# Kernel tuning notes

Hardware: AMD Instinct MI355X
Metric: run time of the kernel (lower is better)

## Reference

```python
import jax, jax.numpy as jnp
import numpy as np

B, T, D = 2, 2048, 2048
NH, HD = 16, 128
Q_LAT, KV_LAT = 1024, 512
EPS = 1e-6
THETA = 10000.0


def setup_inputs() -> dict:
    key = jax.random.key(0)
    ks = jax.random.split(key, 8)
    x = jax.random.normal(ks[0], (B, T, D), dtype=jnp.float32)
    # causal additive mask, broadcast over batch/heads
    neg = jnp.finfo(jnp.float32).min
    causal = jnp.where(jnp.tril(jnp.ones((T, T), dtype=bool)), 0.0, neg)
    attn_mask = causal[None, None, :, :].astype(jnp.float32)
    s = lambda fan_in: 1.0 / np.sqrt(fan_in)
    q_a_w = jax.random.normal(ks[1], (Q_LAT, D), dtype=jnp.float32) * s(D)
    q_b_w = jax.random.normal(ks[2], (NH * HD, Q_LAT), dtype=jnp.float32) * s(Q_LAT)
    kv_a_w = jax.random.normal(ks[3], (KV_LAT, D), dtype=jnp.float32) * s(D)
    k_b_w = jax.random.normal(ks[4], (NH * HD, KV_LAT), dtype=jnp.float32) * s(KV_LAT)
    v_b_w = jax.random.normal(ks[5], (NH * HD, KV_LAT), dtype=jnp.float32) * s(KV_LAT)
    o_w = jax.random.normal(ks[6], (D, NH * HD), dtype=jnp.float32) * s(NH * HD)
    q_norm_w = jnp.ones((HD,), dtype=jnp.float32)
    k_norm_w = jnp.ones((HD,), dtype=jnp.float32)
    return dict(x=x, attn_mask=attn_mask, q_a_w=q_a_w, q_b_w=q_b_w, kv_a_w=kv_a_w,
                k_b_w=k_b_w, v_b_w=v_b_w, o_w=o_w, q_norm_w=q_norm_w, k_norm_w=k_norm_w)


def _rms_norm(x, w):
    var = jnp.mean(jnp.square(x), axis=-1, keepdims=True)
    return x * jax.lax.rsqrt(var + EPS) * w


def _rope_cache(t, hd, dtype):
    inv_freq = 1.0 / (THETA ** (jnp.arange(0, hd, 2, dtype=jnp.float32) / hd))
    freqs = jnp.arange(t, dtype=jnp.float32)[:, None] * inv_freq[None, :]  # [t, hd/2]
    emb = jnp.concatenate([freqs, freqs], axis=-1)  # [t, hd]
    return jnp.cos(emb).astype(dtype), jnp.sin(emb).astype(dtype)


def _rotate_half(x):
    h = x.shape[-1] // 2
    return jnp.concatenate([-x[..., h:], x[..., :h]], axis=-1)


def reference(x, attn_mask, q_a_w, q_b_w, kv_a_w, k_b_w, v_b_w, o_w, q_norm_w, k_norm_w):
    b, t, d = x.shape
    # low-rank projections (torch Linear: y = x @ W.T)
    q = (x @ q_a_w.T) @ q_b_w.T          # [b, t, nh*hd]
    kv = x @ kv_a_w.T                     # [b, t, kv_lat]
    k = kv @ k_b_w.T
    v = kv @ v_b_w.T
    q = q.reshape(b, t, NH, HD).transpose(0, 2, 1, 3)  # [b, nh, t, hd]
    k = k.reshape(b, t, NH, HD).transpose(0, 2, 1, 3)
    v = v.reshape(b, t, NH, HD).transpose(0, 2, 1, 3)
    # QK-norm over head dim
    q = _rms_norm(q, q_norm_w)
    k = _rms_norm(k, k_norm_w)
    # RoPE
    cos, sin = _rope_cache(t, HD, x.dtype)  # [t, hd]
    cos = cos[None, None, :, :]
    sin = sin[None, None, :, :]
    q = q * cos + _rotate_half(q) * sin
    k = k * cos + _rotate_half(k) * sin
    # attention
    sd = 1.0 / np.sqrt(HD)
    attn = jnp.einsum('bhqd,bhkd->bhqk', q, k) * sd + attn_mask
    attn = jax.nn.softmax(attn, axis=-1)
    out = jnp.einsum('bhqk,bhkd->bhqd', attn, v)
    out = out.transpose(0, 2, 1, 3).reshape(b, t, NH * HD)
    return out @ o_w.T
```

## Files before the change

kernel.cpp:

```cpp
#include <hip/hip_runtime.h>
#include <hip/hip_fp16.h>

typedef _Float16 f16;
typedef _Float16 f16x4 __attribute__((ext_vector_type(4)));
typedef _Float16 f16x8 __attribute__((ext_vector_type(8)));
typedef float f32x4 __attribute__((ext_vector_type(4)));

#define BT 4096
#define DMODEL 2048

__device__ __forceinline__ void gld16(const f16* g, f16* l) {
    __builtin_amdgcn_global_load_lds((const __attribute__((address_space(1))) void*)g,
                                     (__attribute__((address_space(3))) void*)l, 16, 0, 0);
}

struct Cvt7 {
    const float* s[7];
    f16* d[7];
    int off4[8];
};
__global__ __launch_bounds__(256) void k_cvt7(Cvt7 c) {
    int i = blockIdx.x * 256 + threadIdx.x;
    if (i >= c.off4[7]) return;
    int seg = 0;
#pragma unroll
    for (int k = 1; k < 7; ++k) seg += (i >= c.off4[k]);
    int j = i - c.off4[seg];
    float4 v = ((const float4*)c.s[seg])[j];
    f16x4 h;
    h[0] = (f16)v.x; h[1] = (f16)v.y; h[2] = (f16)v.z; h[3] = (f16)v.w;
    ((f16x4*)c.d[seg])[j] = h;
}

template <typename CT>
__global__ __launch_bounds__(256, 3) void k_gemm_bt(const f16* __restrict__ A,
                                                    const f16* __restrict__ Bm,
                                                    CT* __restrict__ C,
                                                    int M, int N, int K) {
    __shared__ __align__(16) char smem[16384];
    f16* Als = (f16*)smem;
    f16* Bls = (f16*)(smem + 8192);
    const int tid = threadIdx.x;
    const int w = tid >> 6, l = tid & 63;
    const int quad = l >> 4, ln = l & 15;
    const int m0 = blockIdx.y * 128, n0 = blockIdx.x * 128;
    const int wm = (w >> 1) * 64, wn = (w & 1) * 64;
    const int srow = l >> 2, scol = (l & 3) * 8;

    f32x4 acc[4][4];
#pragma unroll
    for (int i = 0; i < 4; ++i)
#pragma unroll
        for (int j = 0; j < 4; ++j)
#pragma unroll
            for (int r = 0; r < 4; ++r) acc[i][j][r] = 0.f;

    for (int k0 = 0; k0 < K; k0 += 32) {
#pragma unroll
        for (int c = 0; c < 2; ++c) {
            const int ch = w + 4 * c;
            gld16(A + (size_t)(m0 + ch * 16 + srow) * K + (k0 + scol), &Als[ch * 512]);
            gld16(Bm + (size_t)(n0 + ch * 16 + srow) * K + (k0 + scol), &Bls[ch * 512]);
        }
        __syncthreads();
        f16x8 af[4], bf[4];
#pragma unroll
        for (int i = 0; i < 4; ++i) af[i] = *(const f16x8*)&Als[(wm + 16 * i + ln) * 32 + quad * 8];
#pragma unroll
        for (int j = 0; j < 4; ++j) bf[j] = *(const f16x8*)&Bls[(wn + 16 * j + ln) * 32 + quad * 8];
#pragma unroll
        for (int i = 0; i < 4; ++i)
#pragma unroll
            for (int j = 0; j < 4; ++j)
                acc[i][j] = __builtin_amdgcn_mfma_f32_16x16x32_f16(af[i], bf[j], acc[i][j], 0, 0, 0);
        __syncthreads();
    }
    const int p_w = (w >> 1) ? 16 : 0;
#pragma unroll
    for (int i = 0; i < 4; ++i) {
        if constexpr (sizeof(CT) == 2) {
            f16* Cs = (f16*)smem;
#pragma unroll
            for (int j = 0; j < 4; ++j)
#pragma unroll
                for (int r = 0; r < 4; ++r)
                    Cs[(p_w + quad * 4 + r) * 136 + wn + 16 * j + ln] = (f16)acc[i][j][r];
            __syncthreads();
#pragma unroll
            for (int k2 = 0; k2 < 2; ++k2) {
                int idx = k2 * 256 + tid;
                int pr = idx >> 4, c = idx & 15;
                int rg = m0 + 16 * i + (pr & 15) + ((pr & 16) ? 64 : 0);
                *(f16x8*)&C[(size_t)rg * N + n0 + c * 8] = *(const f16x8*)&Cs[pr * 136 + c * 8];
            }
        } else {
            float* Cs = (float*)smem;
#pragma unroll
            for (int j = 0; j < 4; ++j)
#pragma unroll
                for (int r = 0; r < 4; ++r)
                    Cs[(p_w + quad * 4 + r) * 128 + wn + 16 * j + ln] = acc[i][j][r];
            __syncthreads();
#pragma unroll
            for (int k2 = 0; k2 < 4; ++k2) {
                int idx = k2 * 256 + tid;
                int pr = idx >> 5, c = idx & 31;
                int rg = m0 + 16 * i + (pr & 15) + ((pr & 16) ? 64 : 0);
                *(float4*)&C[(size_t)rg * N + n0 + c * 4] = *(const float4*)&Cs[pr * 128 + c * 4];
            }
        }
        __syncthreads();
    }
}

__global__ __launch_bounds__(256, 3) void k_gemm_dual(const f16* __restrict__ A,
                                                      const f16* __restrict__ B0,
                                                      const f16* __restrict__ B1,
                                                      f16* __restrict__ C0, f16* __restrict__ C1,
                                                      int K, int nsplit, int ld0, int ld1) {
    __shared__ __align__(16) char smem[16384];
    f16* Als = (f16*)smem;
    f16* Bls = (f16*)(smem + 8192);
    const int tid = threadIdx.x;
    const int w = tid >> 6, l = tid & 63;
    const int quad = l >> 4, ln = l & 15;
    const int m0 = blockIdx.y * 128, n0 = blockIdx.x * 128;
    const int wm = (w >> 1) * 64, wn = (w & 1) * 64;
    const int srow = l >> 2, scol = (l & 3) * 8;
    const f16* Bm = (n0 < nsplit) ? B0 + (size_t)n0 * K : B1 + (size_t)(n0 - nsplit) * K;

    f32x4 acc[4][4];
#pragma unroll
    for (int i = 0; i < 4; ++i)
#pragma unroll
        for (int j = 0; j < 4; ++j)
#pragma unroll
            for (int r = 0; r < 4; ++r) acc[i][j][r] = 0.f;

    for (int k0 = 0; k0 < K; k0 += 32) {
#pragma unroll
        for (int c = 0; c < 2; ++c) {
            const int ch = w + 4 * c;
            gld16(A + (size_t)(m0 + ch * 16 + srow) * K + (k0 + scol), &Als[ch * 512]);
            gld16(Bm + (size_t)(ch * 16 + srow) * K + (k0 + scol), &Bls[ch * 512]);
        }
        __syncthreads();
        f16x8 af[4], bf[4];
#pragma unroll
        for (int i = 0; i < 4; ++i) af[i] = *(const f16x8*)&Als[(wm + 16 * i + ln) * 32 + quad * 8];
#pragma unroll
        for (int j = 0; j < 4; ++j) bf[j] = *(const f16x8*)&Bls[(wn + 16 * j + ln) * 32 + quad * 8];
#pragma unroll
        for (int i = 0; i < 4; ++i)
#pragma unroll
            for (int j = 0; j < 4; ++j)
                acc[i][j] = __builtin_amdgcn_mfma_f32_16x16x32_f16(af[i], bf[j], acc[i][j], 0, 0, 0);
        __syncthreads();
    }
    f16* Cd; int ldc, cb;
    if (n0 < nsplit) { Cd = C0; ldc = ld0; cb = n0; }
    else             { Cd = C1; ldc = ld1; cb = n0 - nsplit; }
    const int p_w = (w >> 1) ? 16 : 0;
    f16* Cs = (f16*)smem;
#pragma unroll
    for (int i = 0; i < 4; ++i) {
#pragma unroll
        for (int j = 0; j < 4; ++j)
#pragma unroll
            for (int r = 0; r < 4; ++r)
                Cs[(p_w + quad * 4 + r) * 136 + wn + 16 * j + ln] = (f16)acc[i][j][r];
        __syncthreads();
#pragma unroll
        for (int k2 = 0; k2 < 2; ++k2) {
            int idx = k2 * 256 + tid;
            int pr = idx >> 4, c = idx & 15;
            int rg = m0 + 16 * i + (pr & 15) + ((pr & 16) ? 64 : 0);
            *(f16x8*)&Cd[(size_t)rg * ldc + cb + c * 8] = *(const f16x8*)&Cs[pr * 136 + c * 8];
        }
        __syncthreads();
    }
}

__global__ __launch_bounds__(256, 3) void k_gemm_kv(const f16* __restrict__ A,
                                                    const f16* __restrict__ B0,
                                                    const f16* __restrict__ B1,
                                                    f16* __restrict__ Ck, f16* __restrict__ Vt,
                                                    int K) {
    __shared__ __align__(16) char smem[16384];
    f16* Als = (f16*)smem;
    f16* Bls = (f16*)(smem + 8192);
    const int tid = threadIdx.x;
    const int w = tid >> 6, l = tid & 63;
    const int quad = l >> 4, ln = l & 15;
    const int m0 = blockIdx.y * 128, n0 = blockIdx.x * 128;
    const int wm = (w >> 1) * 64, wn = (w & 1) * 64;
    const int srow = l >> 2, scol = (l & 3) * 8;
    const f16* Bm = (n0 < 2048) ? B0 + (size_t)n0 * K : B1 + (size_t)(n0 - 2048) * K;

    f32x4 acc[4][4];
#pragma unroll
    for (int i = 0; i < 4; ++i)
#pragma unroll
        for (int j = 0; j < 4; ++j)
#pragma unroll
            for (int r = 0; r < 4; ++r) acc[i][j][r] = 0.f;

    for (int k0 = 0; k0 < K; k0 += 32) {
#pragma unroll
        for (int c = 0; c < 2; ++c) {
            const int ch = w + 4 * c;
            gld16(A + (size_t)(m0 + ch * 16 + srow) * K + (k0 + scol), &Als[ch * 512]);
            gld16(Bm + (size_t)(ch * 16 + srow) * K + (k0 + scol), &Bls[ch * 512]);
        }
        __syncthreads();
        f16x8 af[4], bf[4];
#pragma unroll
        for (int i = 0; i < 4; ++i) af[i] = *(const f16x8*)&Als[(wm + 16 * i + ln) * 32 + quad * 8];
#pragma unroll
        for (int j = 0; j < 4; ++j) bf[j] = *(const f16x8*)&Bls[(wn + 16 * j + ln) * 32 + quad * 8];
#pragma unroll
        for (int i = 0; i < 4; ++i)
#pragma unroll
            for (int j = 0; j < 4; ++j)
                acc[i][j] = __builtin_amdgcn_mfma_f32_16x16x32_f16(af[i], bf[j], acc[i][j], 0, 0, 0);
        __syncthreads();
    }
    const int p_w = (w >> 1) ? 16 : 0;
    f16* Cs = (f16*)smem;
    const int bb = m0 >> 11;
    const int tb = m0 & 2047;
#pragma unroll
    for (int i = 0; i < 4; ++i) {
#pragma unroll
        for (int j = 0; j < 4; ++j)
#pragma unroll
            for (int r = 0; r < 4; ++r)
                Cs[(p_w + quad * 4 + r) * 136 + wn + 16 * j + ln] = (f16)acc[i][j][r];
        __syncthreads();
        if (n0 < 2048) {
#pragma unroll
            for (int k2 = 0; k2 < 2; ++k2) {
                int idx = k2 * 256 + tid;
                int pr = idx >> 4, c = idx & 15;
                int rg = m0 + 16 * i + (pr & 15) + ((pr & 16) ? 64 : 0);
                *(f16x8*)&Ck[(size_t)rg * 2048 + n0 + c * 8] = *(const f16x8*)&Cs[pr * 136 + c * 8];
            }
        } else {
#pragma unroll
            for (int it = 0; it < 2; ++it) {
                int idx = it * 256 + tid;
                int d = idx & 127, tc = (idx >> 7) & 1, g = idx >> 8;
                f16x8 v;
#pragma unroll
                for (int k = 0; k < 8; ++k) v[k] = Cs[(g * 16 + tc * 8 + k) * 136 + d];
                int t = tb + 16 * i + g * 64 + tc * 8;
                *(f16x8*)&Vt[((size_t)(bb * 2048 + (n0 - 2048) + d)) * 2048 + t] = v;
            }
        }
        __syncthreads();
    }
}

__global__ __launch_bounds__(256) void k_norm_rope(f16* __restrict__ q, f16* __restrict__ k,
                                                   const float* __restrict__ qw,
                                                   const float* __restrict__ kw) {
    const int gw = blockIdx.x * 4 + (threadIdx.x >> 6);
    const int l = threadIdx.x & 63;
    const int which = gw >> 16;
    const int rh = gw & 65535;
    const int row = rh >> 4, h = rh & 15;
    f16* p = which ? k : q;
    const float* wp = which ? kw : qw;
    const float scale = which ? 1.0f : 0.08838834764831843f;
    const size_t base = (size_t)row * DMODEL + h * 128;
    float xa = (float)p[base + l];
    float xb = (float)p[base + 64 + l];
    float ss = xa * xa + xb * xb;
#pragma unroll
    for (int off = 32; off > 0; off >>= 1) ss += __shfl_xor(ss, off);
    const float rms = rsqrtf(ss * (1.0f / 128.0f) + 1e-6f);
    const float na = xa * rms * wp[l];
    const float nb = xb * rms * wp[64 + l];
    const int t = row & 2047;
    const float freq = __expf((float)l * -0.1439115683121279f);
    const float ang = (float)t * freq;
    const float c = cosf(ang), s = sinf(ang);
    p[base + l]      = (f16)((na * c - nb * s) * scale);
    p[base + 64 + l] = (f16)((nb * c + na * s) * scale);
}

__global__ __launch_bounds__(256, 3) void k_flash(const f16* __restrict__ Q, const f16* __restrict__ K,
                                                  const f16* __restrict__ Vt, f16* __restrict__ O) {
    __shared__ f16 Kl[64 * 136];
    __shared__ f16 Vl[128 * 72];
    const int h = blockIdx.x, b = blockIdx.y, mt = 31 - blockIdx.z;
    const int tid = threadIdx.x, w = tid >> 6, l64 = tid & 63;
    const int quad = l64 >> 4, ln = l64 & 15;

    f16x8 qf[4];
    {
        const int tq = mt * 64 + w * 16 + ln;
        const f16* qp = Q + (size_t)(b * 2048 + tq) * DMODEL + h * 128 + quad * 8;
#pragma unroll
        for (int kc = 0; kc < 4; ++kc) qf[kc] = *(const f16x8*)(qp + kc * 32);
    }
    f32x4 oacc[8];
#pragma unroll
    for (int ot = 0; ot < 8; ++ot)
#pragma unroll
        for (int r = 0; r < 4; ++r) oacc[ot][r] = 0.f;
    float m_r = -INFINITY, l_r = 0.f;

    const f16* kbase = K + (size_t)(b * 2048) * DMODEL + h * 128;
    const f16* vbase = Vt + (size_t)(b * 2048 + h * 128) * 2048;

    f16x8 kr[4], vr[4];
#pragma unroll
    for (int c = 0; c < 4; ++c) {
        int idx = c * 256 + tid;
        kr[c] = *(const f16x8*)(kbase + (size_t)(idx >> 4) * DMODEL + (idx & 15) * 8);
        vr[c] = *(const f16x8*)(vbase + (size_t)(idx >> 3) * 2048 + (idx & 7) * 8);
    }

    for (int j = 0; j <= mt; ++j) {
        __syncthreads();
#pragma unroll
        for (int c = 0; c < 4; ++c) {
            int idx = c * 256 + tid;
            *(f16x8*)&Kl[(idx >> 4) * 136 + (idx & 15) * 8] = kr[c];
            *(f16x8*)&Vl[(idx >> 3) * 72 + (idx & 7) * 8] = vr[c];
        }
        __syncthreads();
        if (j < mt) {
#pragma unroll
            for (int c = 0; c < 4; ++c) {
                int idx = c * 256 + tid;
                kr[c] = *(const f16x8*)(kbase + (size_t)((j + 1) * 64 + (idx >> 4)) * DMODEL + (idx & 15) * 8);
                vr[c] = *(const f16x8*)(vbase + (size_t)(idx >> 3) * 2048 + (j + 1) * 64 + (idx & 7) * 8);
            }
        }
        f32x4 sacc[4];
#pragma unroll
        for (int nt = 0; nt < 4; ++nt)
#pragma unroll
            for (int r = 0; r < 4; ++r) sacc[nt][r] = 0.f;
#pragma unroll
        for (int nt = 0; nt < 4; ++nt)
#pragma unroll
            for (int kc = 0; kc < 4; ++kc) {
                f16x8 kf = *(const f16x8*)&Kl[(nt * 16 + ln) * 136 + kc * 32 + quad * 8];
                sacc[nt] = __builtin_amdgcn_mfma_f32_16x16x32_f16(kf, qf[kc], sacc[nt], 0, 0, 0);
            }
        if (j == mt) {
#pragma unroll
            for (int nt = 0; nt < 4; ++nt)
#pragma unroll
                for (int r = 0; r < 4; ++r)
                    if (nt * 16 + quad * 4 + r > w * 16 + ln) sacc[nt][r] = -INFINITY;
        }
        float mx = -INFINITY;
#pragma unroll
        for (int nt = 0; nt < 4; ++nt)
#pragma unroll
            for (int r = 0; r < 4; ++r) mx = fmaxf(mx, sacc[nt][r]);
        mx = fmaxf(mx, __shfl_xor(mx, 16));
        mx = fmaxf(mx, __shfl_xor(mx, 32));
        const float mn = fmaxf(m_r, mx);
        const float alpha = __expf(m_r - mn);
        m_r = mn;
        f16x4 pa[4];
        float s0 = 0.f;
#pragma unroll
        for (int nt = 0; nt < 4; ++nt)
#pragma unroll
            for (int r = 0; r < 4; ++r) {
                float pv = __expf(sacc[nt][r] - mn);
                s0 += pv;
                pa[nt][r] = (f16)pv;
            }
        s0 += __shfl_xor(s0, 16);
        s0 += __shfl_xor(s0, 32);
        l_r = l_r * alpha + s0;
        float ar[4];
#pragma unroll
        for (int r = 0; r < 4; ++r) ar[r] = __shfl(alpha, (l64 & 48) | (quad * 4 + r));
#pragma unroll
        for (int ot = 0; ot < 8; ++ot)
#pragma unroll
            for (int r = 0; r < 4; ++r) oacc[ot][r] *= ar[r];
#pragma unroll
        for (int nt = 0; nt < 4; ++nt)
#pragma unroll
            for (int ot = 0; ot < 8; ++ot) {
                f16x4 vf = *(const f16x4*)&Vl[(ot * 16 + ln) * 72 + nt * 16 + quad * 4];
                oacc[ot] = __builtin_amdgcn_mfma_f32_16x16x16f16(pa[nt], vf, oacc[ot], 0, 0, 0);
            }
    }
    const float inv = 1.0f / l_r;
    float ivr[4];
#pragma unroll
    for (int r = 0; r < 4; ++r) ivr[r] = __shfl(inv, (l64 & 48) | (quad * 4 + r));
    __syncthreads();
#pragma unroll
    for (int ot = 0; ot < 8; ++ot)
#pragma unroll
        for (int r = 0; r < 4; ++r)
            Kl[(w * 16 + quad * 4 + r) * 136 + ot * 16 + ln] = (f16)(oacc[ot][r] * ivr[r]);
    __syncthreads();
#pragma unroll
    for (int c = 0; c < 4; ++c) {
        int idx = c * 256 + tid;
        int row = idx >> 4, col8 = (idx & 15) * 8;
        *(f16x8*)&O[(size_t)(b * 2048 + mt * 64 + row) * DMODEL + h * 128 + col8] =
            *(const f16x8*)&Kl[row * 136 + col8];
    }
}

extern "C" void kernel_launch(void* const* d_in, const int* in_sizes, int n_in,
                              void* d_out, int out_size, void* d_ws, size_t ws_size,
                              hipStream_t stream) {
    const float* x    = (const float*)d_in[0];
    const float* qaw  = (const float*)d_in[2];
    const float* qbw  = (const float*)d_in[3];
    const float* kvaw = (const float*)d_in[4];
    const float* kbw  = (const float*)d_in[5];
    const float* vbw  = (const float*)d_in[6];
    const float* ow   = (const float*)d_in[7];
    const float* qnw  = (const float*)d_in[8];
    const float* knw  = (const float*)d_in[9];
    float* out = (float*)d_out;

    char* p = (char*)d_ws;
    auto alloc = [&](size_t elems) { f16* r = (f16*)p; p += elems * sizeof(f16); return r; };
    f16* xb   = alloc((size_t)BT * 2048);
    f16* wo   = alloc((size_t)2048 * 2048);
    f16* wqa  = alloc((size_t)1024 * 2048);
    f16* wqb  = alloc((size_t)2048 * 1024);
    f16* wkva = alloc((size_t)512 * 2048);
    f16* wkb  = alloc((size_t)2048 * 512);
    f16* wvb  = alloc((size_t)2048 * 512);
    f16* qlat = alloc((size_t)BT * 1024);
    f16* kvb  = alloc((size_t)BT * 512);
    f16* qpre = alloc((size_t)BT * 2048);
    f16* kpre = alloc((size_t)BT * 2048);
    f16* vt   = xb;
    f16* attn = wqa;

    Cvt7 c;
    c.s[0] = x;    c.d[0] = xb;
    c.s[1] = qaw;  c.d[1] = wqa;
    c.s[2] = qbw;  c.d[2] = wqb;
    c.s[3] = kvaw; c.d[3] = wkva;
    c.s[4] = kbw;  c.d[4] = wkb;
    c.s[5] = vbw;  c.d[5] = wvb;
    c.s[6] = ow;   c.d[6] = wo;
    int sz4[7] = {BT * 2048 / 4, 1024 * 2048 / 4, 2048 * 1024 / 4, 512 * 2048 / 4,
                  2048 * 512 / 4, 2048 * 512 / 4, 2048 * 2048 / 4};
    c.off4[0] = 0;
    for (int i = 0; i < 7; ++i) c.off4[i + 1] = c.off4[i] + sz4[i];
    k_cvt7<<<(c.off4[7] + 255) / 256, 256, 0, stream>>>(c);

    dim3 blk(256);
    k_gemm_dual<<<dim3(1536 / 128, BT / 128), blk, 0, stream>>>(xb, wqa, wkva, qlat, kvb, 2048, 1024, 1024, 512);
    k_gemm_bt<f16><<<dim3(2048 / 128, BT / 128), blk, 0, stream>>>(qlat, wqb, qpre, BT, 2048, 1024);
    k_gemm_kv<<<dim3(4096 / 128, BT / 128), blk, 0, stream>>>(kvb, wkb, wvb, kpre, vt, 512);
    k_norm_rope<<<32768, 256, 0, stream>>>(qpre, kpre, qnw, knw);
    k_flash<<<dim3(16, 2, 32), 256, 0, stream>>>(qpre, kpre, vt, attn);
    k_gemm_bt<float><<<dim3(2048 / 128, BT / 128), blk, 0, stream>>>(attn, wo, out, BT, 2048, 2048);
}
```

Measured before the change: 389.9 us.

## Merge Q-up and KV-up GEMMs into one launch, vectorize norm-rope, use exp2 softmax

Folds the q_b projection GEMM and the k/v up-projection GEMM into a single kernel launch that picks operands by block region, which removes a launch and fills the GPU better with one larger grid. The norm+RoPE kernel now uses 32 lanes per head, each doing four-wide vector loads and stores, and gets the rotate-half partner through a lane shuffle. The query scale now carries a log2(e) factor so the flash kernel can use exp2f instead of __expf. The mixed-K grid can leave load imbalance between blocks with K=1024 and blocks with K=512.

```diff
diff --git a/kernel.cpp b/kernel.cpp
--- a/kernel.cpp
+++ b/kernel.cpp
@@ -181,21 +181,33 @@
     }
 }
 
-__global__ __launch_bounds__(256, 3) void k_gemm_kv(const f16* __restrict__ A,
-                                                    const f16* __restrict__ B0,
-                                                    const f16* __restrict__ B1,
-                                                    f16* __restrict__ Ck, f16* __restrict__ Vt,
-                                                    int K) {
+__global__ __launch_bounds__(256, 3) void k_gemm3(const f16* __restrict__ qlat,
+                                                  const f16* __restrict__ kvb,
+                                                  const f16* __restrict__ wqb,
+                                                  const f16* __restrict__ wkb,
+                                                  const f16* __restrict__ wvb,
+                                                  f16* __restrict__ qpre,
+                                                  f16* __restrict__ kpre,
+                                                  f16* __restrict__ vt) {
     __shared__ __align__(16) char smem[16384];
     f16* Als = (f16*)smem;
     f16* Bls = (f16*)(smem + 8192);
     const int tid = threadIdx.x;
     const int w = tid >> 6, l = tid & 63;
     const int quad = l >> 4, ln = l & 15;
-    const int m0 = blockIdx.y * 128, n0 = blockIdx.x * 128;
+    const int m0 = blockIdx.y * 128;
+    const int bx = blockIdx.x;
+    const int region = bx >> 4;
+    const int n0 = (bx & 15) * 128;
     const int wm = (w >> 1) * 64, wn = (w & 1) * 64;
     const int srow = l >> 2, scol = (l & 3) * 8;
-    const f16* Bm = (n0 < 2048) ? B0 + (size_t)n0 * K : B1 + (size_t)(n0 - 2048) * K;
+
+    const f16* A;
+    const f16* Bm;
+    int K;
+    if (region == 0)      { A = qlat; Bm = wqb + (size_t)n0 * 1024; K = 1024; }
+    else if (region == 1) { A = kvb;  Bm = wkb + (size_t)n0 * 512;  K = 512; }
+    else                  { A = kvb;  Bm = wvb + (size_t)n0 * 512;  K = 512; }
 
     f32x4 acc[4][4];
 #pragma unroll
@@ -227,8 +239,7 @@
     }
     const int p_w = (w >> 1) ? 16 : 0;
     f16* Cs = (f16*)smem;
-    const int bb = m0 >> 11;
-    const int tb = m0 & 2047;
+    const int bb = m0 >> 11, tb = m0 & 2047;
 #pragma unroll
     for (int i = 0; i < 4; ++i) {
 #pragma unroll
@@ -237,13 +248,14 @@
             for (int r = 0; r < 4; ++r)
                 Cs[(p_w + quad * 4 + r) * 136 + wn + 16 * j + ln] = (f16)acc[i][j][r];
         __syncthreads();
-        if (n0 < 2048) {
+        if (region < 2) {
+            f16* Cd = region ? kpre : qpre;
 #pragma unroll
             for (int k2 = 0; k2 < 2; ++k2) {
                 int idx = k2 * 256 + tid;
                 int pr = idx >> 4, c = idx & 15;
                 int rg = m0 + 16 * i + (pr & 15) + ((pr & 16) ? 64 : 0);
-                *(f16x8*)&Ck[(size_t)rg * 2048 + n0 + c * 8] = *(const f16x8*)&Cs[pr * 136 + c * 8];
+                *(f16x8*)&Cd[(size_t)rg * 2048 + n0 + c * 8] = *(const f16x8*)&Cs[pr * 136 + c * 8];
             }
         } else {
 #pragma unroll
@@ -254,7 +266,7 @@
 #pragma unroll
                 for (int k = 0; k < 8; ++k) v[k] = Cs[(g * 16 + tc * 8 + k) * 136 + d];
                 int t = tb + 16 * i + g * 64 + tc * 8;
-                *(f16x8*)&Vt[((size_t)(bb * 2048 + (n0 - 2048) + d)) * 2048 + t] = v;
+                *(f16x8*)&vt[((size_t)(bb * 2048 + n0 + d)) * 2048 + t] = v;
             }
         }
         __syncthreads();
@@ -264,29 +276,37 @@
 __global__ __launch_bounds__(256) void k_norm_rope(f16* __restrict__ q, f16* __restrict__ k,
                                                    const float* __restrict__ qw,
                                                    const float* __restrict__ kw) {
-    const int gw = blockIdx.x * 4 + (threadIdx.x >> 6);
-    const int l = threadIdx.x & 63;
-    const int which = gw >> 16;
-    const int rh = gw & 65535;
+    const int tid = threadIdx.x;
+    const int id = blockIdx.x * 8 + (tid >> 5);
+    const int j = tid & 31;
+    const int which = id >> 16;
+    const int rh = id & 65535;
     const int row = rh >> 4, h = rh & 15;
     f16* p = which ? k : q;
     const float* wp = which ? kw : qw;
-    const float scale = which ? 1.0f : 0.08838834764831843f;
+    const float scale = which ? 1.0f : 0.12751743f;
     const size_t base = (size_t)row * DMODEL + h * 128;
-    float xa = (float)p[base + l];
-    float xb = (float)p[base + 64 + l];
-    float ss = xa * xa + xb * xb;
-#pragma unroll
-    for (int off = 32; off > 0; off >>= 1) ss += __shfl_xor(ss, off);
+    f16x4 xv = *(const f16x4*)&p[base + 4 * j];
+    float x0 = (float)xv[0], x1 = (float)xv[1], x2 = (float)xv[2], x3 = (float)xv[3];
+    float ss = x0 * x0 + x1 * x1 + x2 * x2 + x3 * x3;
+#pragma unroll
+    for (int off = 16; off > 0; off >>= 1) ss += __shfl_xor(ss, off);
     const float rms = rsqrtf(ss * (1.0f / 128.0f) + 1e-6f);
-    const float na = xa * rms * wp[l];
-    const float nb = xb * rms * wp[64 + l];
+    float4 wv = *(const float4*)&wp[4 * j];
+    float n0 = x0 * rms * wv.x, n1 = x1 * rms * wv.y, n2 = x2 * rms * wv.z, n3 = x3 * rms * wv.w;
+    float p0 = __shfl_xor(n0, 16), p1 = __shfl_xor(n1, 16), p2 = __shfl_xor(n2, 16), p3 = __shfl_xor(n3, 16);
     const int t = row & 2047;
-    const float freq = __expf((float)l * -0.1439115683121279f);
-    const float ang = (float)t * freq;
-    const float c = cosf(ang), s = sinf(ang);
-    p[base + l]      = (f16)((na * c - nb * s) * scale);
-    p[base + 64 + l] = (f16)((nb * c + na * s) * scale);
+    const float sgn = (j < 16) ? -1.f : 1.f;
+    const int fi = (4 * j) & 63;
+    float nv[4] = {n0, n1, n2, n3}, pv[4] = {p0, p1, p2, p3};
+    f16x4 o;
+#pragma unroll
+    for (int c = 0; c < 4; ++c) {
+        const float fr = exp2f(-0.20762051f * (float)(fi + c));
+        const float ang = (float)t * fr;
+        o[c] = (f16)((nv[c] * cosf(ang) + sgn * pv[c] * sinf(ang)) * scale);
+    }
+    *(f16x4*)&p[base + 4 * j] = o;
 }
 
 __global__ __launch_bounds__(256, 3) void k_flash(const f16* __restrict__ Q, const f16* __restrict__ K,
@@ -366,7 +386,7 @@
         mx = fmaxf(mx, __shfl_xor(mx, 16));
         mx = fmaxf(mx, __shfl_xor(mx, 32));
         const float mn = fmaxf(m_r, mx);
-        const float alpha = __expf(m_r - mn);
+        const float alpha = exp2f(m_r - mn);
         m_r = mn;
         f16x4 pa[4];
         float s0 = 0.f;
@@ -374,7 +394,7 @@
         for (int nt = 0; nt < 4; ++nt)
 #pragma unroll
             for (int r = 0; r < 4; ++r) {
-                float pv = __expf(sacc[nt][r] - mn);
+                float pv = exp2f(sacc[nt][r] - mn);
                 s0 += pv;
                 pa[nt][r] = (f16)pv;
             }
@@ -462,9 +482,8 @@
 
     dim3 blk(256);
     k_gemm_dual<<<dim3(1536 / 128, BT / 128), blk, 0, stream>>>(xb, wqa, wkva, qlat, kvb, 2048, 1024, 1024, 512);
-    k_gemm_bt<f16><<<dim3(2048 / 128, BT / 128), blk, 0, stream>>>(qlat, wqb, qpre, BT, 2048, 1024);
-    k_gemm_kv<<<dim3(4096 / 128, BT / 128), blk, 0, stream>>>(kvb, wkb, wvb, kpre, vt, 512);
-    k_norm_rope<<<32768, 256, 0, stream>>>(qpre, kpre, qnw, knw);
+    k_gemm3<<<dim3(48, BT / 128), blk, 0, stream>>>(qlat, kvb, wqb, wkb, wvb, qpre, kpre, vt);
+    k_norm_rope<<<16384, 256, 0, stream>>>(qpre, kpre, qnw, knw);
     k_flash<<<dim3(16, 2, 32), 256, 0, stream>>>(qpre, kpre, vt, attn);
     k_gemm_bt<float><<<dim3(2048 / 128, BT / 128), blk, 0, stream>>>(attn, wo, out, BT, 2048, 2048);
 }
```

Result: slower. 407.2 us (+4.5%).
